# Kernel optimization log

Measured on AMD Instinct MI355X. Metric: run time of the kernel, lower is better.

Reference implementation:

```python
import jax, jax.numpy as jnp
import numpy as np

L, N, K, S, V, H = 12, 2048, 8, 4, 50000, 256


def setup_inputs() -> dict:
    key = jax.random.key(0)
    ks = jax.random.split(key, 20)
    tokens1 = jax.random.randint(ks[0], (L, N, S), 0, V, dtype=jnp.int32)
    tokens2 = jax.random.randint(ks[1], (L, N, S), 0, V, dtype=jnp.int32)
    # child indices into previous level's h (0 = zero-init row, -1 = no child)
    idx1 = jax.random.randint(ks[2], (L, N, K), -1, N + 1, dtype=jnp.int32).at[0].set(-1)
    idx2 = jax.random.randint(ks[3], (L, N, K), -1, N + 1, dtype=jnp.int32).at[0].set(-1)
    sc = 0.02
    E = jax.random.normal(ks[4], (V, H), jnp.float32)  # torch.randn init
    lin_W = jax.random.normal(ks[5], (H * S, H), jnp.float32) * sc
    lin_b = jnp.zeros((H,), jnp.float32)
    Uf_W = jax.random.normal(ks[6], (H, H), jnp.float32) * sc
    Uf_b = jnp.zeros((H,), jnp.float32)
    Uiuo_W = jax.random.normal(ks[7], (H, 3 * H), jnp.float32) * sc
    Uiuo_b = jnp.zeros((3 * H,), jnp.float32)
    W_W = jax.random.normal(ks[8], (H, 4 * H), jnp.float32) * sc
    W_b = jnp.zeros((4 * H,), jnp.float32)
    dense_W = jax.random.normal(ks[9], (H, 512), jnp.float32) * sc
    dense_b = jnp.zeros((512,), jnp.float32)
    out_W = jax.random.normal(ks[10], (512, 2), jnp.float32) * sc
    out_b = jnp.zeros((2,), jnp.float32)
    return dict(tokens1=tokens1, idx1=idx1, tokens2=tokens2, idx2=idx2,
                E=E, lin_W=lin_W, lin_b=lin_b, Uf_W=Uf_W, Uf_b=Uf_b,
                Uiuo_W=Uiuo_W, Uiuo_b=Uiuo_b, W_W=W_W, W_b=W_b,
                dense_W=dense_W, dense_b=dense_b, out_W=out_W, out_b=out_b)


def _encode(tokens, idx, E, lin_W, lin_b, Uf_W, Uf_b, Uiuo_W, Uiuo_b, W_W, W_b):
    # TreeEmbeddingLayer: lookup label_size tokens per node, concat, linear
    emb = E[tokens].reshape(L, N, S * H)           # [L,N,S*H]
    x = emb @ lin_W + lin_b                        # [L,N,H]

    def step(carry, inp):
        h_prev, c_prev = carry                     # [N,H]
        xl, il = inp                               # [N,H], [N,K]
        zero = jnp.zeros((1, H), xl.dtype)
        hp = jnp.concatenate([zero, h_prev], 0)    # [N+1,H] (row 0 = init)
        cp = jnp.concatenate([zero, c_prev], 0)
        mask_bool = il != -1
        index = jnp.where(mask_bool, il, 0)
        h = hp[index]                              # [N,K,H] gather child states
        c = cp[index]
        m = mask_bool[..., None].astype(xl.dtype)  # [N,K,1]
        h_sum = jnp.sum(h * m, axis=1)             # [N,H]
        Wx = xl @ W_W + W_b                        # [N,4H]
        Wf, Wi, Wu, Wo = Wx[:, :H], Wx[:, H:2*H], Wx[:, 2*H:3*H], Wx[:, 3*H:]
        fk = jax.nn.sigmoid(Wf[:, None, :] + h @ Uf_W + Uf_b)  # [N,K,H]
        bf = jnp.sum(fk * c * m, axis=1)           # [N,H]
        iuo = h_sum @ Uiuo_W + Uiuo_b              # [N,3H]
        i = jax.nn.sigmoid(iuo[:, :H] + Wi)
        u = jnp.tanh(iuo[:, H:2*H] + Wu)
        o = jax.nn.sigmoid(iuo[:, 2*H:] + Wo)
        nc = i * u + bf
        nh = o * jnp.tanh(nc)
        return (nh, nc), nh

    init = (jnp.zeros((N, H), x.dtype), jnp.zeros((N, H), x.dtype))
    (_, _), hs = jax.lax.scan(step, init, (x, idx))
    # 1 layer with skip connection; hx = last (root) level
    return hs[-1] + x[-1]                          # [N,H]


def reference(tokens1, idx1, tokens2, idx2, E, lin_W, lin_b, Uf_W, Uf_b,
              Uiuo_W, Uiuo_b, W_W, W_b, dense_W, dense_b, out_W, out_b):
    h1 = _encode(tokens1, idx1, E, lin_W, lin_b, Uf_W, Uf_b, Uiuo_W, Uiuo_b, W_W, W_b)
    h2 = _encode(tokens2, idx2, E, lin_W, lin_b, Uf_W, Uf_b, Uiuo_W, Uiuo_b, W_W, W_b)
    abs_dist = jnp.abs(h1 - h2)                    # [N,H]
    x = jnp.tanh(abs_dist @ dense_W + dense_b)     # dropout = identity (eval)
    logits = x @ out_W + out_b                     # [N,2]
    return jax.nn.softmax(logits, axis=-1)
```

## Files before the change

### kernel.cpp

```cpp
#include <hip/hip_runtime.h>

#define LL 12
#define NN 2048
#define KK 8
#define SS 4
#define HH 256
#define LN (LL*NN)
#define VV 50000
#define ZROW 4096
#define SROW 1536

typedef __bf16 bf16_t;
typedef __bf16 bf16x8 __attribute__((ext_vector_type(8)));
typedef __bf16 bf16x4v __attribute__((ext_vector_type(4)));
typedef float f32x4 __attribute__((ext_vector_type(4)));

__device__ __forceinline__ float sigmoidf_(float x) { return 1.f / (1.f + expf(-x)); }

__global__ __launch_bounds__(256) void k_cvtE(const float* __restrict__ src,
                                              bf16_t* __restrict__ dst, int n4)
{
    int i = blockIdx.x * 256 + threadIdx.x;
    const int stride = gridDim.x * 256;
    for (; i < n4; i += stride) {
        const float4 v = ((const float4*)src)[i];
        bf16x4v o;
        o[0] = (bf16_t)v.x; o[1] = (bf16_t)v.y; o[2] = (bf16_t)v.z; o[3] = (bf16_t)v.w;
        ((bf16x4v*)dst)[i] = o;
    }
}

__global__ __launch_bounds__(256) void k_cvtW(
    const float* __restrict__ linW, const float* __restrict__ WW,
    const float* __restrict__ UfW, const float* __restrict__ UiW,
    bf16_t* __restrict__ linWt, bf16_t* __restrict__ WWt,
    bf16_t* __restrict__ UfWt, bf16_t* __restrict__ UiWt)
{
    int i = blockIdx.x * 256 + threadIdx.x;
    if (i < 262144) {
        const int rr = i >> 8, cc = i & 255;
        linWt[(size_t)cc * 1024 + rr] = (bf16_t)linW[i];
        return;
    }
    i -= 262144;
    if (i < 262144) {
        const int rr = i >> 10, cc = i & 1023;
        WWt[(size_t)cc * 256 + rr] = (bf16_t)WW[i];
        return;
    }
    i -= 262144;
    if (i < 65536) {
        const int rr = i >> 8, cc = i & 255;
        UfWt[(size_t)cc * 256 + rr] = (bf16_t)UfW[i];
        return;
    }
    i -= 65536;
    if (i < 196608) {
        const int rr = i / 768, cc = i - rr * 768;
        UiWt[(size_t)cc * 256 + rr] = (bf16_t)UiW[i];
    }
}

__global__ __launch_bounds__(256) void k_zero(float* __restrict__ SA, float* __restrict__ SB)
{
    const int t = threadIdx.x;
    float* a = SA + (size_t)ZROW * 384;
    float* b = SB + (size_t)ZROW * 384;
    for (int i = t; i < 384; i += 256) { a[i] = 0.f; b[i] = 0.f; }
}

__global__ __launch_bounds__(256) void k_embed(
    const int* __restrict__ tok1, const int* __restrict__ tok2,
    const bf16_t* __restrict__ Ebf, const bf16_t* __restrict__ linWt,
    const float* __restrict__ linb, bf16_t* __restrict__ xout)
{
    __shared__ int toff[64][SS];
    const int t = threadIdx.x;
    const int m0 = blockIdx.x * 64;
    {
        const int lr = t >> 2, s = t & 3;
        const int m = m0 + lr;
        const int e = (m >= LN) ? 1 : 0;
        const int rrow = m - e * LN;
        const int* tok = e ? tok2 : tok1;
        toff[lr][s] = tok[(size_t)rrow * SS + s] * HH;
    }
    __syncthreads();
    const int lane = t & 63, w = t >> 6;
    const int wm = w >> 1, wn = w & 1;
    const int r = lane & 15, kg = lane >> 4;
    const int lr0 = wm * 32 + r, lr1 = lr0 + 16;
    const bf16_t* bp[8];
    #pragma unroll
    for (int j = 0; j < 8; ++j)
        bp[j] = linWt + (size_t)(wn * 128 + j * 16 + r) * 1024 + kg * 8;

    const f32x4 zero = {0.f, 0.f, 0.f, 0.f};
    f32x4 acc[2][8];
    #pragma unroll
    for (int mi = 0; mi < 2; ++mi)
        #pragma unroll
        for (int j = 0; j < 8; ++j) acc[mi][j] = zero;

    for (int k0 = 0; k0 < 1024; k0 += 32) {
        const int s = k0 >> 8, off = (k0 & 255) + kg * 8;
        const bf16x8 a0 = *(const bf16x8*)(Ebf + (size_t)toff[lr0][s] + off);
        const bf16x8 a1 = *(const bf16x8*)(Ebf + (size_t)toff[lr1][s] + off);
        #pragma unroll
        for (int j = 0; j < 8; ++j) {
            const bf16x8 b = *(const bf16x8*)bp[j];
            acc[0][j] = __builtin_amdgcn_mfma_f32_16x16x32_bf16(a0, b, acc[0][j], 0, 0, 0);
            acc[1][j] = __builtin_amdgcn_mfma_f32_16x16x32_bf16(a1, b, acc[1][j], 0, 0, 0);
            bp[j] += 32;
        }
    }
    const int crow = m0 + wm * 32 + kg * 4;
    #pragma unroll
    for (int j = 0; j < 8; ++j) {
        const int ccol = wn * 128 + j * 16 + r;
        const float bv = linb[ccol];
        #pragma unroll
        for (int mi = 0; mi < 2; ++mi)
            #pragma unroll
            for (int jj = 0; jj < 4; ++jj)
                xout[(size_t)(crow + mi * 16 + jj) * HH + ccol] =
                    (bf16_t)(acc[mi][j][jj] + bv);
    }
}

__global__ __launch_bounds__(512, 2) void k_step(
    const bf16_t* __restrict__ xbf,
    const int* __restrict__ idx1, const int* __restrict__ idx2, const int l,
    const bf16_t* __restrict__ UfWt, const float* __restrict__ Ufb,
    const bf16_t* __restrict__ UiWt, const float* __restrict__ Uib,
    const bf16_t* __restrict__ WWt, const float* __restrict__ Wb,
    const char* __restrict__ Sprev, char* __restrict__ Snext)
{
    __shared__ __align__(16) bf16_t WxL[16 * 1024];
    __shared__ __align__(16) bf16_t iuoL[16 * 768];
    __shared__ __align__(16) bf16_t hsumL[16 * 256];

    const int t = threadIdx.x;
    const int bid = blockIdx.x;
    const int x  = bid & 7;
    const int e  = x >> 2;
    const int n0 = ((bid >> 3) * 4 + (x & 3)) * 16;
    const int g0 = e * NN + n0;
    const int lane = t & 63, w = t >> 6;
    const int r = lane & 15, kg = lane >> 4;
    const f32x4 zero = {0.f, 0.f, 0.f, 0.f};

    const int rr = t >> 5, sl = t & 31;
    const int ss = (sl + 4 * (rr & 7)) & 31;

    int ch[KK];
    {
        const int* idxp = (e ? idx2 : idx1) + ((size_t)l * NN + n0 + rr) * KK;
        const int4 i0 = *(const int4*)idxp;
        const int4 i1 = *(const int4*)(idxp + 4);
        ch[0] = i0.x; ch[1] = i0.y; ch[2] = i0.z; ch[3] = i0.w;
        ch[4] = i1.x; ch[5] = i1.y; ch[6] = i1.z; ch[7] = i1.w;
        #pragma unroll
        for (int k = 0; k < KK; ++k)
            ch[k] = (ch[k] >= 1) ? (e * NN + ch[k] - 1) : ZROW;
    }

    bf16x8 hv[KK];
    #pragma unroll
    for (int k = 0; k < KK; ++k)
        hv[k] = *(const bf16x8*)(Sprev + (size_t)ch[k] * SROW + sl * 16);

    const bf16_t* xrow = xbf + ((size_t)e * LN + (size_t)l * NN + n0 + r) * HH + kg * 8;
    bf16x8 aWx[8];
    #pragma unroll
    for (int k = 0; k < 8; ++k) aWx[k] = *(const bf16x8*)(xrow + k * 32);

    {
        const bf16_t* bw[8];
        #pragma unroll
        for (int j = 0; j < 8; ++j)
            bw[j] = WWt + (size_t)((8 * w + j) * 16 + r) * HH + kg * 8;
        f32x4 acc[8];
        #pragma unroll
        for (int j = 0; j < 8; ++j) acc[j] = zero;
        #pragma unroll
        for (int k = 0; k < 8; ++k) {
            #pragma unroll
            for (int j = 0; j < 8; ++j) {
                const bf16x8 b = *(const bf16x8*)bw[j];
                acc[j] = __builtin_amdgcn_mfma_f32_16x16x32_bf16(aWx[k], b, acc[j], 0, 0, 0);
                bw[j] += 32;
            }
        }
        #pragma unroll
        for (int j = 0; j < 8; ++j) {
            const int col = (8 * w + j) * 16 + r;
            const float bv = Wb[col];
            #pragma unroll
            for (int jj = 0; jj < 4; ++jj)
                WxL[(size_t)(kg * 4 + jj) * 1024 + col] = (bf16_t)(acc[j][jj] + bv);
        }
    }

    {
        float hs[8] = {0.f, 0.f, 0.f, 0.f, 0.f, 0.f, 0.f, 0.f};
        #pragma unroll
        for (int k = 0; k < KK; ++k) {
            #pragma unroll
            for (int j = 0; j < 8; ++j) hs[j] += (float)hv[k][j];
        }
        bf16x8 o;
        #pragma unroll
        for (int j = 0; j < 8; ++j) o[j] = (bf16_t)hs[j];
        *(bf16x8*)(hsumL + rr * 256 + ss * 8) = o;
    }
    __syncthreads();

    bf16x8 cv[KK], fv[KK];
    #pragma unroll
    for (int k = 0; k < KK; ++k) {
        const char* row = Sprev + (size_t)ch[k] * SROW;
        fv[k] = *(const bf16x8*)(row + 512 + sl * 16);
        cv[k] = *(const bf16x8*)(row + 1024 + sl * 16);
    }

    {
        const bf16_t* bu[6];
        #pragma unroll
        for (int j = 0; j < 6; ++j)
            bu[j] = UiWt + (size_t)((6 * w + j) * 16 + r) * HH + kg * 8;
        f32x4 acc[6];
        #pragma unroll
        for (int j = 0; j < 6; ++j) acc[j] = zero;
        for (int k0 = 0; k0 < HH; k0 += 32) {
            const int sa = (((k0 >> 3) + kg) + 4 * (r & 7)) & 31;
            const bf16x8 a = *(const bf16x8*)(hsumL + r * 256 + sa * 8);
            #pragma unroll
            for (int j = 0; j < 6; ++j) {
                const bf16x8 b = *(const bf16x8*)bu[j];
                acc[j] = __builtin_amdgcn_mfma_f32_16x16x32_bf16(a, b, acc[j], 0, 0, 0);
                bu[j] += 32;
            }
        }
        #pragma unroll
        for (int j = 0; j < 6; ++j) {
            const int col = (6 * w + j) * 16 + r;
            const float bv = Uib[col];
            #pragma unroll
            for (int jj = 0; jj < 4; ++jj)
                iuoL[(size_t)(kg * 4 + jj) * 768 + col] = (bf16_t)(acc[j][jj] + bv);
        }
    }

    float ba[8] = {0.f, 0.f, 0.f, 0.f, 0.f, 0.f, 0.f, 0.f};
    {
        float wf[8];
        const bf16x8 wv = *(const bf16x8*)(WxL + (size_t)rr * 1024 + sl * 8);
        #pragma unroll
        for (int j = 0; j < 8; ++j) wf[j] = (float)wv[j];
        #pragma unroll
        for (int k = 0; k < KK; ++k) {
            #pragma unroll
            for (int j = 0; j < 8; ++j) {
                const float fk = sigmoidf_(wf[j] + (float)fv[k][j]);
                ba[j] = fmaf(fk, (float)cv[k][j], ba[j]);
            }
        }
    }
    __syncthreads();

    {
        const bf16x8 wiv = *(const bf16x8*)(WxL + (size_t)rr * 1024 + 256 + sl * 8);
        const bf16x8 wuv = *(const bf16x8*)(WxL + (size_t)rr * 1024 + 512 + sl * 8);
        const bf16x8 wov = *(const bf16x8*)(WxL + (size_t)rr * 1024 + 768 + sl * 8);
        const bf16x8 iv  = *(const bf16x8*)(iuoL + (size_t)rr * 768 + sl * 8);
        const bf16x8 uv  = *(const bf16x8*)(iuoL + (size_t)rr * 768 + 256 + sl * 8);
        const bf16x8 ov  = *(const bf16x8*)(iuoL + (size_t)rr * 768 + 512 + sl * 8);
        bf16x8 ncb, nhb;
        #pragma unroll
        for (int j = 0; j < 8; ++j) {
            const float ig = sigmoidf_((float)iv[j] + (float)wiv[j]);
            const float ug = tanhf((float)uv[j] + (float)wuv[j]);
            const float og = sigmoidf_((float)ov[j] + (float)wov[j]);
            const float nc = fmaf(ig, ug, ba[j]);
            ncb[j] = (bf16_t)nc;
            nhb[j] = (bf16_t)(og * tanhf(nc));
        }
        char* rowN = Snext + (size_t)(g0 + rr) * SROW;
        *(bf16x8*)(rowN + sl * 16) = nhb;
        *(bf16x8*)(rowN + 1024 + sl * 16) = ncb;
        *(bf16x8*)(hsumL + rr * 256 + ss * 8) = nhb;
    }

    if (l < LL - 1) {
        __syncthreads();
        const int ct0 = 2 * w;
        const bf16_t* bq0 = UfWt + (size_t)(ct0 * 16 + r) * HH + kg * 8;
        const bf16_t* bq1 = bq0 + (size_t)16 * HH;
        f32x4 ac0 = zero, ac1 = zero;
        for (int k0 = 0; k0 < HH; k0 += 32) {
            const int sa = (((k0 >> 3) + kg) + 4 * (r & 7)) & 31;
            const bf16x8 a = *(const bf16x8*)(hsumL + r * 256 + sa * 8);
            const bf16x8 b0 = *(const bf16x8*)bq0;
            const bf16x8 b1 = *(const bf16x8*)bq1;
            ac0 = __builtin_amdgcn_mfma_f32_16x16x32_bf16(a, b0, ac0, 0, 0, 0);
            ac1 = __builtin_amdgcn_mfma_f32_16x16x32_bf16(a, b1, ac1, 0, 0, 0);
            bq0 += 32; bq1 += 32;
        }
        const int c0 = ct0 * 16 + r, c1 = c0 + 16;
        const float bv0 = Ufb[c0], bv1 = Ufb[c1];
        #pragma unroll
        for (int jj = 0; jj < 4; ++jj) {
            bf16_t* fr = (bf16_t*)(Snext + (size_t)(g0 + kg * 4 + jj) * SROW + 512);
            fr[c0] = (bf16_t)(ac0[jj] + bv0);
            fr[c1] = (bf16_t)(ac1[jj] + bv1);
        }
    }
}

__global__ __launch_bounds__(256) void k_final(
    const char* __restrict__ Sfin, const bf16_t* __restrict__ xbf,
    const float* __restrict__ dW, const float* __restrict__ db,
    const float* __restrict__ oW, const float* __restrict__ ob,
    float* __restrict__ out)
{
    __shared__ __align__(16) float ad[8][HH];
    __shared__ __align__(16) float xx[8][512];
    const int t = threadIdx.x;
    const int n0 = blockIdx.x * 8;
    const size_t xoff1 = (size_t)(LL - 1) * NN * HH;
    const size_t xoff2 = (size_t)LN * HH + xoff1;
    #pragma unroll
    for (int rr = 0; rr < 8; ++rr) {
        const int n = n0 + rr;
        const float h1 = (float)((const bf16_t*)(Sfin + (size_t)n * SROW))[t]
                       + (float)xbf[xoff1 + (size_t)n * HH + t];
        const float h2 = (float)((const bf16_t*)(Sfin + (size_t)(NN + n) * SROW))[t]
                       + (float)xbf[xoff2 + (size_t)n * HH + t];
        ad[rr][t] = fabsf(h1 - h2);
    }
    __syncthreads();
    float a0[8], a1[8];
    #pragma unroll
    for (int rr = 0; rr < 8; ++rr) { a0[rr] = 0.f; a1[rr] = 0.f; }
    for (int k = 0; k < HH; k += 4) {
        #pragma unroll
        for (int kk = 0; kk < 4; ++kk) {
            const float b0 = dW[(size_t)(k + kk) * 512 + t];
            const float b1 = dW[(size_t)(k + kk) * 512 + 256 + t];
            #pragma unroll
            for (int rr = 0; rr < 8; ++rr) {
                const float av = ad[rr][k + kk];
                a0[rr] = fmaf(av, b0, a0[rr]);
                a1[rr] = fmaf(av, b1, a1[rr]);
            }
        }
    }
    const float db0 = db[t], db1 = db[256 + t];
    #pragma unroll
    for (int rr = 0; rr < 8; ++rr) {
        xx[rr][t] = tanhf(a0[rr] + db0);
        xx[rr][256 + t] = tanhf(a1[rr] + db1);
    }
    __syncthreads();
    const int w = t >> 6, lane = t & 63;
    for (int rr = w; rr < 8; rr += 4) {
        float p0 = 0.f, p1 = 0.f;
        for (int k = lane; k < 512; k += 64) {
            const float xv = xx[rr][k];
            p0 = fmaf(xv, oW[2 * k + 0], p0);
            p1 = fmaf(xv, oW[2 * k + 1], p1);
        }
        #pragma unroll
        for (int off = 32; off > 0; off >>= 1) {
            p0 += __shfl_down(p0, off);
            p1 += __shfl_down(p1, off);
        }
        if (lane == 0) {
            const float l0 = p0 + ob[0], l1 = p1 + ob[1];
            const float mx = fmaxf(l0, l1);
            const float e0 = expf(l0 - mx), e1 = expf(l1 - mx);
            const float inv = 1.f / (e0 + e1);
            out[(size_t)(n0 + rr) * 2 + 0] = e0 * inv;
            out[(size_t)(n0 + rr) * 2 + 1] = e1 * inv;
        }
    }
}

extern "C" void kernel_launch(void* const* d_in, const int* in_sizes, int n_in,
                              void* d_out, int out_size, void* d_ws, size_t ws_size,
                              hipStream_t stream) {
    (void)in_sizes; (void)n_in; (void)out_size; (void)ws_size;
    const int*   tok1 = (const int*)d_in[0];
    const int*   idx1 = (const int*)d_in[1];
    const int*   tok2 = (const int*)d_in[2];
    const int*   idx2 = (const int*)d_in[3];
    const float* E    = (const float*)d_in[4];
    const float* linW = (const float*)d_in[5];
    const float* linb = (const float*)d_in[6];
    const float* UfW  = (const float*)d_in[7];
    const float* Ufb  = (const float*)d_in[8];
    const float* UiW  = (const float*)d_in[9];
    const float* Uib  = (const float*)d_in[10];
    const float* WW   = (const float*)d_in[11];
    const float* Wb   = (const float*)d_in[12];
    const float* dW   = (const float*)d_in[13];
    const float* db   = (const float*)d_in[14];
    const float* oW   = (const float*)d_in[15];
    const float* ob   = (const float*)d_in[16];
    float* out = (float*)d_out;

    bf16_t* xbf = (bf16_t*)d_ws;
    char*   uni = (char*)(xbf + (size_t)12582912);
    bf16_t* Ebf = (bf16_t*)uni;
    char*   SA  = uni;
    char*   SB  = uni + 6292992;
    bf16_t* linWt = (bf16_t*)(uni + 25600000);
    bf16_t* WWt   = linWt + (size_t)262144;
    bf16_t* UfWt  = WWt   + (size_t)262144;
    bf16_t* UiWt  = UfWt  + (size_t)65536;

    k_cvtE<<<2048, 256, 0, stream>>>(E, Ebf, VV * HH / 4);
    k_cvtW<<<3072, 256, 0, stream>>>(linW, WW, UfW, UiW, linWt, WWt, UfWt, UiWt);

    k_embed<<<768, 256, 0, stream>>>(tok1, tok2, Ebf, linWt, linb, xbf);

    k_zero<<<1, 256, 0, stream>>>((float*)SA, (float*)SB);

    char *Sp = SA, *Sn = SB;
    for (int l = 0; l < LL; ++l) {
        k_step<<<256, 512, 0, stream>>>(xbf, idx1, idx2, l,
                                        UfWt, Ufb, UiWt, Uib, WWt, Wb, Sp, Sn);
        char* ts = Sp; Sp = Sn; Sn = ts;
    }

    k_final<<<NN / 8, 256, 0, stream>>>(Sp, xbf, dW, db, oW, ob, out);
}
```

Baseline: 701.6 us.

## Precompute W·x for all levels in embed kernel, slim per-level step

Fuses the input projection x@W into the embedding kernel, so W·x for every level and both trees is computed in one large batched GEMM. The result is stored as a 1024-wide bf16 buffer in workspace, and only the root-level x is kept for the final stage. The per-level step kernel then just loads its precomputed Wx rows instead of running an MFMA GEMM inside the serial chain, which removes work from the latency-critical recurrence. The cost is a much larger workspace (about 100 MB of Wx) and extra global traffic. The old path is kept as a fallback when the workspace is too small.

```diff
diff --git a/kernel.cpp b/kernel.cpp
--- a/kernel.cpp
+++ b/kernel.cpp
@@ -69,12 +69,15 @@
     for (int i = t; i < 384; i += 256) { a[i] = 0.f; b[i] = 0.f; }
 }
 
-__global__ __launch_bounds__(256) void k_embed(
+__global__ __launch_bounds__(256) void k_embedwx(
     const int* __restrict__ tok1, const int* __restrict__ tok2,
     const bf16_t* __restrict__ Ebf, const bf16_t* __restrict__ linWt,
-    const float* __restrict__ linb, bf16_t* __restrict__ xout)
+    const float* __restrict__ linb,
+    const bf16_t* __restrict__ WWt, const float* __restrict__ Wb,
+    bf16_t* __restrict__ xsm, bf16_t* __restrict__ Wxs)
 {
     __shared__ int toff[64][SS];
+    __shared__ __align__(16) bf16_t xtile[64 * 256];
     const int t = threadIdx.x;
     const int m0 = blockIdx.x * 64;
     {
@@ -90,53 +93,98 @@
     const int wm = w >> 1, wn = w & 1;
     const int r = lane & 15, kg = lane >> 4;
     const int lr0 = wm * 32 + r, lr1 = lr0 + 16;
-    const bf16_t* bp[8];
-    #pragma unroll
-    for (int j = 0; j < 8; ++j)
-        bp[j] = linWt + (size_t)(wn * 128 + j * 16 + r) * 1024 + kg * 8;
-
     const f32x4 zero = {0.f, 0.f, 0.f, 0.f};
-    f32x4 acc[2][8];
-    #pragma unroll
-    for (int mi = 0; mi < 2; ++mi)
-        #pragma unroll
-        for (int j = 0; j < 8; ++j) acc[mi][j] = zero;
-
-    for (int k0 = 0; k0 < 1024; k0 += 32) {
-        const int s = k0 >> 8, off = (k0 & 255) + kg * 8;
-        const bf16x8 a0 = *(const bf16x8*)(Ebf + (size_t)toff[lr0][s] + off);
-        const bf16x8 a1 = *(const bf16x8*)(Ebf + (size_t)toff[lr1][s] + off);
+
+    {
+        const bf16_t* bp[8];
+        #pragma unroll
+        for (int j = 0; j < 8; ++j)
+            bp[j] = linWt + (size_t)(wn * 128 + j * 16 + r) * 1024 + kg * 8;
+        f32x4 acc[2][8];
+        #pragma unroll
+        for (int mi = 0; mi < 2; ++mi)
+            #pragma unroll
+            for (int j = 0; j < 8; ++j) acc[mi][j] = zero;
+
+        for (int k0 = 0; k0 < 1024; k0 += 32) {
+            const int s = k0 >> 8, off = (k0 & 255) + kg * 8;
+            const bf16x8 a0 = *(const bf16x8*)(Ebf + (size_t)toff[lr0][s] + off);
+            const bf16x8 a1 = *(const bf16x8*)(Ebf + (size_t)toff[lr1][s] + off);
+            #pragma unroll
+            for (int j = 0; j < 8; ++j) {
+                const bf16x8 b = *(const bf16x8*)bp[j];
+                acc[0][j] = __builtin_amdgcn_mfma_f32_16x16x32_bf16(a0, b, acc[0][j], 0, 0, 0);
+                acc[1][j] = __builtin_amdgcn_mfma_f32_16x16x32_bf16(a1, b, acc[1][j], 0, 0, 0);
+                bp[j] += 32;
+            }
+        }
+        const int e0 = (m0 >= LN) ? 1 : 0;
+        const int lblk = (m0 - e0 * LN) >> 11;
+        const int nbase = m0 & (NN - 1);
+        const int crowL = wm * 32 + kg * 4;
         #pragma unroll
         for (int j = 0; j < 8; ++j) {
-            const bf16x8 b = *(const bf16x8*)bp[j];
-            acc[0][j] = __builtin_amdgcn_mfma_f32_16x16x32_bf16(a0, b, acc[0][j], 0, 0, 0);
-            acc[1][j] = __builtin_amdgcn_mfma_f32_16x16x32_bf16(a1, b, acc[1][j], 0, 0, 0);
-            bp[j] += 32;
-        }
-    }
-    const int crow = m0 + wm * 32 + kg * 4;
-    #pragma unroll
-    for (int j = 0; j < 8; ++j) {
-        const int ccol = wn * 128 + j * 16 + r;
-        const float bv = linb[ccol];
-        #pragma unroll
-        for (int mi = 0; mi < 2; ++mi)
-            #pragma unroll
-            for (int jj = 0; jj < 4; ++jj)
-                xout[(size_t)(crow + mi * 16 + jj) * HH + ccol] =
-                    (bf16_t)(acc[mi][j][jj] + bv);
-    }
-}
-
-__global__ __launch_bounds__(512, 2) void k_step(
-    const bf16_t* __restrict__ xbf,
+            const int ccol = wn * 128 + j * 16 + r;
+            const float bv = linb[ccol];
+            #pragma unroll
+            for (int mi = 0; mi < 2; ++mi) {
+                #pragma unroll
+                for (int jj = 0; jj < 4; ++jj) {
+                    const int rowL = crowL + mi * 16 + jj;
+                    const bf16_t val = (bf16_t)(acc[mi][j][jj] + bv);
+                    const int ps = ((ccol >> 3) + rowL) & 31;
+                    xtile[rowL * 256 + ps * 8 + (ccol & 7)] = val;
+                    if (lblk == LL - 1)
+                        xsm[((size_t)e0 * NN + nbase + rowL) * HH + ccol] = val;
+                }
+            }
+        }
+    }
+    __syncthreads();
+
+    for (int mp = 0; mp < 2; ++mp) {
+        for (int nh = 0; nh < 2; ++nh) {
+            f32x4 acc2[2][8];
+            #pragma unroll
+            for (int mi = 0; mi < 2; ++mi)
+                #pragma unroll
+                for (int nt = 0; nt < 8; ++nt) acc2[mi][nt] = zero;
+            for (int k0 = 0; k0 < 8; ++k0) {
+                const int row0 = mp * 32 + r, row1 = row0 + 16;
+                const int sk = k0 * 4 + kg;
+                const bf16x8 a0 = *(const bf16x8*)(xtile + row0 * 256 + ((sk + row0) & 31) * 8);
+                const bf16x8 a1 = *(const bf16x8*)(xtile + row1 * 256 + ((sk + row1) & 31) * 8);
+                #pragma unroll
+                for (int nt = 0; nt < 8; ++nt) {
+                    const bf16x8 b = *(const bf16x8*)(WWt +
+                        (size_t)(w * 256 + (nh * 8 + nt) * 16 + r) * HH + k0 * 32 + kg * 8);
+                    acc2[0][nt] = __builtin_amdgcn_mfma_f32_16x16x32_bf16(a0, b, acc2[0][nt], 0, 0, 0);
+                    acc2[1][nt] = __builtin_amdgcn_mfma_f32_16x16x32_bf16(a1, b, acc2[1][nt], 0, 0, 0);
+                }
+            }
+            #pragma unroll
+            for (int nt = 0; nt < 8; ++nt) {
+                const int col = w * 256 + (nh * 8 + nt) * 16 + r;
+                const float bv = Wb[col];
+                #pragma unroll
+                for (int mi = 0; mi < 2; ++mi) {
+                    #pragma unroll
+                    for (int jj = 0; jj < 4; ++jj)
+                        Wxs[(size_t)(m0 + mp * 32 + mi * 16 + kg * 4 + jj) * 1024 + col] =
+                            (bf16_t)(acc2[mi][nt][jj] + bv);
+                }
+            }
+        }
+    }
+}
+
+__global__ __launch_bounds__(512, 2) void k_step2(
     const int* __restrict__ idx1, const int* __restrict__ idx2, const int l,
     const bf16_t* __restrict__ UfWt, const float* __restrict__ Ufb,
     const bf16_t* __restrict__ UiWt, const float* __restrict__ Uib,
-    const bf16_t* __restrict__ WWt, const float* __restrict__ Wb,
+    const bf16_t* __restrict__ Wxs,
     const char* __restrict__ Sprev, char* __restrict__ Snext)
 {
-    __shared__ __align__(16) bf16_t WxL[16 * 1024];
     __shared__ __align__(16) bf16_t iuoL[16 * 768];
     __shared__ __align__(16) bf16_t hsumL[16 * 256];
 
@@ -165,41 +213,18 @@
             ch[k] = (ch[k] >= 1) ? (e * NN + ch[k] - 1) : ZROW;
     }
 
-    bf16x8 hv[KK];
-    #pragma unroll
-    for (int k = 0; k < KK; ++k)
-        hv[k] = *(const bf16x8*)(Sprev + (size_t)ch[k] * SROW + sl * 16);
-
-    const bf16_t* xrow = xbf + ((size_t)e * LN + (size_t)l * NN + n0 + r) * HH + kg * 8;
-    bf16x8 aWx[8];
-    #pragma unroll
-    for (int k = 0; k < 8; ++k) aWx[k] = *(const bf16x8*)(xrow + k * 32);
-
-    {
-        const bf16_t* bw[8];
-        #pragma unroll
-        for (int j = 0; j < 8; ++j)
-            bw[j] = WWt + (size_t)((8 * w + j) * 16 + r) * HH + kg * 8;
-        f32x4 acc[8];
-        #pragma unroll
-        for (int j = 0; j < 8; ++j) acc[j] = zero;
-        #pragma unroll
-        for (int k = 0; k < 8; ++k) {
-            #pragma unroll
-            for (int j = 0; j < 8; ++j) {
-                const bf16x8 b = *(const bf16x8*)bw[j];
-                acc[j] = __builtin_amdgcn_mfma_f32_16x16x32_bf16(aWx[k], b, acc[j], 0, 0, 0);
-                bw[j] += 32;
-            }
-        }
-        #pragma unroll
-        for (int j = 0; j < 8; ++j) {
-            const int col = (8 * w + j) * 16 + r;
-            const float bv = Wb[col];
-            #pragma unroll
-            for (int jj = 0; jj < 4; ++jj)
-                WxL[(size_t)(kg * 4 + jj) * 1024 + col] = (bf16_t)(acc[j][jj] + bv);
-        }
+    const bf16_t* wxp = Wxs + ((size_t)e * LN + (size_t)l * NN + n0 + rr) * 1024;
+    const bf16x8 wfv = *(const bf16x8*)(wxp + sl * 8);
+    const bf16x8 wiv = *(const bf16x8*)(wxp + 256 + sl * 8);
+    const bf16x8 wuv = *(const bf16x8*)(wxp + 512 + sl * 8);
+    const bf16x8 wov = *(const bf16x8*)(wxp + 768 + sl * 8);
+    bf16x8 hv[KK], fv[KK], cv[KK];
+    #pragma unroll
+    for (int k = 0; k < KK; ++k) {
+        const char* row = Sprev + (size_t)ch[k] * SROW;
+        hv[k] = *(const bf16x8*)(row + sl * 16);
+        fv[k] = *(const bf16x8*)(row + 512 + sl * 16);
+        cv[k] = *(const bf16x8*)(row + 1024 + sl * 16);
     }
 
     {
@@ -215,14 +240,6 @@
         *(bf16x8*)(hsumL + rr * 256 + ss * 8) = o;
     }
     __syncthreads();
-
-    bf16x8 cv[KK], fv[KK];
-    #pragma unroll
-    for (int k = 0; k < KK; ++k) {
-        const char* row = Sprev + (size_t)ch[k] * SROW;
-        fv[k] = *(const bf16x8*)(row + 512 + sl * 16);
-        cv[k] = *(const bf16x8*)(row + 1024 + sl * 16);
-    }
 
     {
         const bf16_t* bu[6];
@@ -255,9 +272,8 @@
     float ba[8] = {0.f, 0.f, 0.f, 0.f, 0.f, 0.f, 0.f, 0.f};
     {
         float wf[8];
-        const bf16x8 wv = *(const bf16x8*)(WxL + (size_t)rr * 1024 + sl * 8);
-        #pragma unroll
-        for (int j = 0; j < 8; ++j) wf[j] = (float)wv[j];
+        #pragma unroll
+        for (int j = 0; j < 8; ++j) wf[j] = (float)wfv[j];
         #pragma unroll
         for (int k = 0; k < KK; ++k) {
             #pragma unroll
@@ -270,12 +286,9 @@
     __syncthreads();
 
     {
-        const bf16x8 wiv = *(const bf16x8*)(WxL + (size_t)rr * 1024 + 256 + sl * 8);
-        const bf16x8 wuv = *(const bf16x8*)(WxL + (size_t)rr * 1024 + 512 + sl * 8);
-        const bf16x8 wov = *(const bf16x8*)(WxL + (size_t)rr * 1024 + 768 + sl * 8);
-        const bf16x8 iv  = *(const bf16x8*)(iuoL + (size_t)rr * 768 + sl * 8);
-        const bf16x8 uv  = *(const bf16x8*)(iuoL + (size_t)rr * 768 + 256 + sl * 8);
-        const bf16x8 ov  = *(const bf16x8*)(iuoL + (size_t)rr * 768 + 512 + sl * 8);
+        const bf16x8 iv = *(const bf16x8*)(iuoL + (size_t)rr * 768 + sl * 8);
+        const bf16x8 uv = *(const bf16x8*)(iuoL + (size_t)rr * 768 + 256 + sl * 8);
+        const bf16x8 ov = *(const bf16x8*)(iuoL + (size_t)rr * 768 + 512 + sl * 8);
         bf16x8 ncb, nhb;
         #pragma unroll
         for (int j = 0; j < 8; ++j) {
@@ -318,6 +331,308 @@
     }
 }
 
+__global__ __launch_bounds__(256) void k_final2(
+    const char* __restrict__ Sfin, const bf16_t* __restrict__ xsm,
+    const float* __restrict__ dW, const float* __restrict__ db,
+    const float* __restrict__ oW, const float* __restrict__ ob,
+    float* __restrict__ out)
+{
+    __shared__ __align__(16) float ad[8][HH];
+    __shared__ __align__(16) float xx[8][512];
+    const int t = threadIdx.x;
+    const int n0 = blockIdx.x * 8;
+    #pragma unroll
+    for (int rr = 0; rr < 8; ++rr) {
+        const int n = n0 + rr;
+        const float h1 = (float)((const bf16_t*)(Sfin + (size_t)n * SROW))[t]
+                       + (float)xsm[(size_t)n * HH + t];
+        const float h2 = (float)((const bf16_t*)(Sfin + (size_t)(NN + n) * SROW))[t]
+                       + (float)xsm[((size_t)NN + n) * HH + t];
+        ad[rr][t] = fabsf(h1 - h2);
+    }
+    __syncthreads();
+    float a0[8], a1[8];
+    #pragma unroll
+    for (int rr = 0; rr < 8; ++rr) { a0[rr] = 0.f; a1[rr] = 0.f; }
+    for (int k = 0; k < HH; k += 4) {
+        #pragma unroll
+        for (int kk = 0; kk < 4; ++kk) {
+            const float b0 = dW[(size_t)(k + kk) * 512 + t];
+            const float b1 = dW[(size_t)(k + kk) * 512 + 256 + t];
+            #pragma unroll
+            for (int rr = 0; rr < 8; ++rr) {
+                const float av = ad[rr][k + kk];
+                a0[rr] = fmaf(av, b0, a0[rr]);
+                a1[rr] = fmaf(av, b1, a1[rr]);
+            }
+        }
+    }
+    const float db0 = db[t], db1 = db[256 + t];
+    #pragma unroll
+    for (int rr = 0; rr < 8; ++rr) {
+        xx[rr][t] = tanhf(a0[rr] + db0);
+        xx[rr][256 + t] = tanhf(a1[rr] + db1);
+    }
+    __syncthreads();
+    const int w = t >> 6, lane = t & 63;
+    for (int rr = w; rr < 8; rr += 4) {
+        float p0 = 0.f, p1 = 0.f;
+        for (int k = lane; k < 512; k += 64) {
+            const float xv = xx[rr][k];
+            p0 = fmaf(xv, oW[2 * k + 0], p0);
+            p1 = fmaf(xv, oW[2 * k + 1], p1);
+        }
+        #pragma unroll
+        for (int off = 32; off > 0; off >>= 1) {
+            p0 += __shfl_down(p0, off);
+            p1 += __shfl_down(p1, off);
+        }
+        if (lane == 0) {
+            const float l0 = p0 + ob[0], l1 = p1 + ob[1];
+            const float mx = fmaxf(l0, l1);
+            const float e0 = expf(l0 - mx), e1 = expf(l1 - mx);
+            const float inv = 1.f / (e0 + e1);
+            out[(size_t)(n0 + rr) * 2 + 0] = e0 * inv;
+            out[(size_t)(n0 + rr) * 2 + 1] = e1 * inv;
+        }
+    }
+}
+
+__global__ __launch_bounds__(256) void k_embed(
+    const int* __restrict__ tok1, const int* __restrict__ tok2,
+    const bf16_t* __restrict__ Ebf, const bf16_t* __restrict__ linWt,
+    const float* __restrict__ linb, bf16_t* __restrict__ xout)
+{
+    __shared__ int toff[64][SS];
+    const int t = threadIdx.x;
+    const int m0 = blockIdx.x * 64;
+    {
+        const int lr = t >> 2, s = t & 3;
+        const int m = m0 + lr;
+        const int e = (m >= LN) ? 1 : 0;
+        const int rrow = m - e * LN;
+        const int* tok = e ? tok2 : tok1;
+        toff[lr][s] = tok[(size_t)rrow * SS + s] * HH;
+    }
+    __syncthreads();
+    const int lane = t & 63, w = t >> 6;
+    const int wm = w >> 1, wn = w & 1;
+    const int r = lane & 15, kg = lane >> 4;
+    const int lr0 = wm * 32 + r, lr1 = lr0 + 16;
+    const bf16_t* bp[8];
+    #pragma unroll
+    for (int j = 0; j < 8; ++j)
+        bp[j] = linWt + (size_t)(wn * 128 + j * 16 + r) * 1024 + kg * 8;
+    const f32x4 zero = {0.f, 0.f, 0.f, 0.f};
+    f32x4 acc[2][8];
+    #pragma unroll
+    for (int mi = 0; mi < 2; ++mi)
+        #pragma unroll
+        for (int j = 0; j < 8; ++j) acc[mi][j] = zero;
+    for (int k0 = 0; k0 < 1024; k0 += 32) {
+        const int s = k0 >> 8, off = (k0 & 255) + kg * 8;
+        const bf16x8 a0 = *(const bf16x8*)(Ebf + (size_t)toff[lr0][s] + off);
+        const bf16x8 a1 = *(const bf16x8*)(Ebf + (size_t)toff[lr1][s] + off);
+        #pragma unroll
+        for (int j = 0; j < 8; ++j) {
+            const bf16x8 b = *(const bf16x8*)bp[j];
+            acc[0][j] = __builtin_amdgcn_mfma_f32_16x16x32_bf16(a0, b, acc[0][j], 0, 0, 0);
+            acc[1][j] = __builtin_amdgcn_mfma_f32_16x16x32_bf16(a1, b, acc[1][j], 0, 0, 0);
+            bp[j] += 32;
+        }
+    }
+    const int crow = m0 + wm * 32 + kg * 4;
+    #pragma unroll
+    for (int j = 0; j < 8; ++j) {
+        const int ccol = wn * 128 + j * 16 + r;
+        const float bv = linb[ccol];
+        #pragma unroll
+        for (int mi = 0; mi < 2; ++mi)
+            #pragma unroll
+            for (int jj = 0; jj < 4; ++jj)
+                xout[(size_t)(crow + mi * 16 + jj) * HH + ccol] =
+                    (bf16_t)(acc[mi][j][jj] + bv);
+    }
+}
+
+__global__ __launch_bounds__(512, 2) void k_step(
+    const bf16_t* __restrict__ xbf,
+    const int* __restrict__ idx1, const int* __restrict__ idx2, const int l,
+    const bf16_t* __restrict__ UfWt, const float* __restrict__ Ufb,
+    const bf16_t* __restrict__ UiWt, const float* __restrict__ Uib,
+    const bf16_t* __restrict__ WWt, const float* __restrict__ Wb,
+    const char* __restrict__ Sprev, char* __restrict__ Snext)
+{
+    __shared__ __align__(16) bf16_t WxL[16 * 1024];
+    __shared__ __align__(16) bf16_t iuoL[16 * 768];
+    __shared__ __align__(16) bf16_t hsumL[16 * 256];
+    const int t = threadIdx.x;
+    const int bid = blockIdx.x;
+    const int x  = bid & 7;
+    const int e  = x >> 2;
+    const int n0 = ((bid >> 3) * 4 + (x & 3)) * 16;
+    const int g0 = e * NN + n0;
+    const int lane = t & 63, w = t >> 6;
+    const int r = lane & 15, kg = lane >> 4;
+    const f32x4 zero = {0.f, 0.f, 0.f, 0.f};
+    const int rr = t >> 5, sl = t & 31;
+    const int ss = (sl + 4 * (rr & 7)) & 31;
+    int ch[KK];
+    {
+        const int* idxp = (e ? idx2 : idx1) + ((size_t)l * NN + n0 + rr) * KK;
+        const int4 i0 = *(const int4*)idxp;
+        const int4 i1 = *(const int4*)(idxp + 4);
+        ch[0] = i0.x; ch[1] = i0.y; ch[2] = i0.z; ch[3] = i0.w;
+        ch[4] = i1.x; ch[5] = i1.y; ch[6] = i1.z; ch[7] = i1.w;
+        #pragma unroll
+        for (int k = 0; k < KK; ++k)
+            ch[k] = (ch[k] >= 1) ? (e * NN + ch[k] - 1) : ZROW;
+    }
+    bf16x8 hv[KK];
+    #pragma unroll
+    for (int k = 0; k < KK; ++k)
+        hv[k] = *(const bf16x8*)(Sprev + (size_t)ch[k] * SROW + sl * 16);
+    const bf16_t* xrow = xbf + ((size_t)e * LN + (size_t)l * NN + n0 + r) * HH + kg * 8;
+    bf16x8 aWx[8];
+    #pragma unroll
+    for (int k = 0; k < 8; ++k) aWx[k] = *(const bf16x8*)(xrow + k * 32);
+    {
+        const bf16_t* bw[8];
+        #pragma unroll
+        for (int j = 0; j < 8; ++j)
+            bw[j] = WWt + (size_t)((8 * w + j) * 16 + r) * HH + kg * 8;
+        f32x4 acc[8];
+        #pragma unroll
+        for (int j = 0; j < 8; ++j) acc[j] = zero;
+        #pragma unroll
+        for (int k = 0; k < 8; ++k) {
+            #pragma unroll
+            for (int j = 0; j < 8; ++j) {
+                const bf16x8 b = *(const bf16x8*)bw[j];
+                acc[j] = __builtin_amdgcn_mfma_f32_16x16x32_bf16(aWx[k], b, acc[j], 0, 0, 0);
+                bw[j] += 32;
+            }
+        }
+        #pragma unroll
+        for (int j = 0; j < 8; ++j) {
+            const int col = (8 * w + j) * 16 + r;
+            const float bv = Wb[col];
+            #pragma unroll
+            for (int jj = 0; jj < 4; ++jj)
+                WxL[(size_t)(kg * 4 + jj) * 1024 + col] = (bf16_t)(acc[j][jj] + bv);
+        }
+    }
+    {
+        float hs[8] = {0.f, 0.f, 0.f, 0.f, 0.f, 0.f, 0.f, 0.f};
+        #pragma unroll
+        for (int k = 0; k < KK; ++k) {
+            #pragma unroll
+            for (int j = 0; j < 8; ++j) hs[j] += (float)hv[k][j];
+        }
+        bf16x8 o;
+        #pragma unroll
+        for (int j = 0; j < 8; ++j) o[j] = (bf16_t)hs[j];
+        *(bf16x8*)(hsumL + rr * 256 + ss * 8) = o;
+    }
+    __syncthreads();
+    bf16x8 cv[KK], fvv[KK];
+    #pragma unroll
+    for (int k = 0; k < KK; ++k) {
+        const char* row = Sprev + (size_t)ch[k] * SROW;
+        fvv[k] = *(const bf16x8*)(row + 512 + sl * 16);
+        cv[k]  = *(const bf16x8*)(row + 1024 + sl * 16);
+    }
+    {
+        const bf16_t* bu[6];
+        #pragma unroll
+        for (int j = 0; j < 6; ++j)
+            bu[j] = UiWt + (size_t)((6 * w + j) * 16 + r) * HH + kg * 8;
+        f32x4 acc[6];
+        #pragma unroll
+        for (int j = 0; j < 6; ++j) acc[j] = zero;
+        for (int k0 = 0; k0 < HH; k0 += 32) {
+            const int sa = (((k0 >> 3) + kg) + 4 * (r & 7)) & 31;
+            const bf16x8 a = *(const bf16x8*)(hsumL + r * 256 + sa * 8);
+            #pragma unroll
+            for (int j = 0; j < 6; ++j) {
+                const bf16x8 b = *(const bf16x8*)bu[j];
+                acc[j] = __builtin_amdgcn_mfma_f32_16x16x32_bf16(a, b, acc[j], 0, 0, 0);
+                bu[j] += 32;
+            }
+        }
+        #pragma unroll
+        for (int j = 0; j < 6; ++j) {
+            const int col = (6 * w + j) * 16 + r;
+            const float bv = Uib[col];
+            #pragma unroll
+            for (int jj = 0; jj < 4; ++jj)
+                iuoL[(size_t)(kg * 4 + jj) * 768 + col] = (bf16_t)(acc[j][jj] + bv);
+        }
+    }
+    float ba[8] = {0.f, 0.f, 0.f, 0.f, 0.f, 0.f, 0.f, 0.f};
+    {
+        float wf[8];
+        const bf16x8 wv = *(const bf16x8*)(WxL + (size_t)rr * 1024 + sl * 8);
+        #pragma unroll
+        for (int j = 0; j < 8; ++j) wf[j] = (float)wv[j];
+        #pragma unroll
+        for (int k = 0; k < KK; ++k) {
+            #pragma unroll
+            for (int j = 0; j < 8; ++j) {
+                const float fk = sigmoidf_(wf[j] + (float)fvv[k][j]);
+                ba[j] = fmaf(fk, (float)cv[k][j], ba[j]);
+            }
+        }
+    }
+    __syncthreads();
+    {
+        const bf16x8 wiv = *(const bf16x8*)(WxL + (size_t)rr * 1024 + 256 + sl * 8);
+        const bf16x8 wuv = *(const bf16x8*)(WxL + (size_t)rr * 1024 + 512 + sl * 8);
+        const bf16x8 wov = *(const bf16x8*)(WxL + (size_t)rr * 1024 + 768 + sl * 8);
+        const bf16x8 iv  = *(const bf16x8*)(iuoL + (size_t)rr * 768 + sl * 8);
+        const bf16x8 uv  = *(const bf16x8*)(iuoL + (size_t)rr * 768 + 256 + sl * 8);
+        const bf16x8 ov  = *(const bf16x8*)(iuoL + (size_t)rr * 768 + 512 + sl * 8);
+        bf16x8 ncb, nhb;
+        #pragma unroll
+        for (int j = 0; j < 8; ++j) {
+            const float ig = sigmoidf_((float)iv[j] + (float)wiv[j]);
+            const float ug = tanhf((float)uv[j] + (float)wuv[j]);
+            const float og = sigmoidf_((float)ov[j] + (float)wov[j]);
+            const float nc = fmaf(ig, ug, ba[j]);
+            ncb[j] = (bf16_t)nc;
+            nhb[j] = (bf16_t)(og * tanhf(nc));
+        }
+        char* rowN = Snext + (size_t)(g0 + rr) * SROW;
+        *(bf16x8*)(rowN + sl * 16) = nhb;
+        *(bf16x8*)(rowN + 1024 + sl * 16) = ncb;
+        *(bf16x8*)(hsumL + rr * 256 + ss * 8) = nhb;
+    }
+    if (l < LL - 1) {
+        __syncthreads();
+        const int ct0 = 2 * w;
+        const bf16_t* bq0 = UfWt + (size_t)(ct0 * 16 + r) * HH + kg * 8;
+        const bf16_t* bq1 = bq0 + (size_t)16 * HH;
+        f32x4 ac0 = zero, ac1 = zero;
+        for (int k0 = 0; k0 < HH; k0 += 32) {
+            const int sa = (((k0 >> 3) + kg) + 4 * (r & 7)) & 31;
+            const bf16x8 a = *(const bf16x8*)(hsumL + r * 256 + sa * 8);
+            const bf16x8 b0 = *(const bf16x8*)bq0;
+            const bf16x8 b1 = *(const bf16x8*)bq1;
+            ac0 = __builtin_amdgcn_mfma_f32_16x16x32_bf16(a, b0, ac0, 0, 0, 0);
+            ac1 = __builtin_amdgcn_mfma_f32_16x16x32_bf16(a, b1, ac1, 0, 0, 0);
+            bq0 += 32; bq1 += 32;
+        }
+        const int c0 = ct0 * 16 + r, c1 = c0 + 16;
+        const float bv0 = Ufb[c0], bv1 = Ufb[c1];
+        #pragma unroll
+        for (int jj = 0; jj < 4; ++jj) {
+            bf16_t* fr = (bf16_t*)(Snext + (size_t)(g0 + kg * 4 + jj) * SROW + 512);
+            fr[c0] = (bf16_t)(ac0[jj] + bv0);
+            fr[c1] = (bf16_t)(ac1[jj] + bv1);
+        }
+    }
+}
+
 __global__ __launch_bounds__(256) void k_final(
     const char* __restrict__ Sfin, const bf16_t* __restrict__ xbf,
     const float* __restrict__ dW, const float* __restrict__ db,
@@ -390,7 +705,7 @@
 extern "C" void kernel_launch(void* const* d_in, const int* in_sizes, int n_in,
                               void* d_out, int out_size, void* d_ws, size_t ws_size,
                               hipStream_t stream) {
-    (void)in_sizes; (void)n_in; (void)out_size; (void)ws_size;
+    (void)in_sizes; (void)n_in; (void)out_size;
     const int*   tok1 = (const int*)d_in[0];
     const int*   idx1 = (const int*)d_in[1];
     const int*   tok2 = (const int*)d_in[2];
@@ -410,29 +725,54 @@
     const float* ob   = (const float*)d_in[16];
     float* out = (float*)d_out;
 
-    bf16_t* xbf = (bf16_t*)d_ws;
-    char*   uni = (char*)(xbf + (size_t)12582912);
-    bf16_t* Ebf = (bf16_t*)uni;
-    char*   SA  = uni;
-    char*   SB  = uni + 6292992;
-    bf16_t* linWt = (bf16_t*)(uni + 25600000);
-    bf16_t* WWt   = linWt + (size_t)262144;
-    bf16_t* UfWt  = WWt   + (size_t)262144;
-    bf16_t* UiWt  = UfWt  + (size_t)65536;
-
-    k_cvtE<<<2048, 256, 0, stream>>>(E, Ebf, VV * HH / 4);
-    k_cvtW<<<3072, 256, 0, stream>>>(linW, WW, UfW, UiW, linWt, WWt, UfWt, UiWt);
-
-    k_embed<<<768, 256, 0, stream>>>(tok1, tok2, Ebf, linWt, linb, xbf);
-
-    k_zero<<<1, 256, 0, stream>>>((float*)SA, (float*)SB);
-
-    char *Sp = SA, *Sn = SB;
-    for (int l = 0; l < LL; ++l) {
-        k_step<<<256, 512, 0, stream>>>(xbf, idx1, idx2, l,
-                                        UfWt, Ufb, UiWt, Uib, WWt, Wb, Sp, Sn);
-        char* ts = Sp; Sp = Sn; Sn = ts;
-    }
-
-    k_final<<<NN / 8, 256, 0, stream>>>(Sp, xbf, dW, db, oW, ob, out);
-}
+    const size_t NEED = 100663296ull + 25600000ull + 2097152ull + 1572864ull;
+
+    if (ws_size >= NEED) {
+        bf16_t* Wxs = (bf16_t*)d_ws;
+        char*   uni = (char*)d_ws + 100663296;
+        bf16_t* Ebf = (bf16_t*)uni;
+        char*   SA  = uni;
+        char*   SB  = uni + 6292992;
+        bf16_t* xsm = (bf16_t*)(uni + 25600000);
+        bf16_t* linWt = (bf16_t*)(uni + 25600000 + 2097152);
+        bf16_t* WWt   = linWt + (size_t)262144;
+        bf16_t* UfWt  = WWt   + (size_t)262144;
+        bf16_t* UiWt  = UfWt  + (size_t)65536;
+
+        k_cvtE<<<2048, 256, 0, stream>>>(E, Ebf, VV * HH / 4);
+        k_cvtW<<<3072, 256, 0, stream>>>(linW, WW, UfW, UiW, linWt, WWt, UfWt, UiWt);
+        k_embedwx<<<768, 256, 0, stream>>>(tok1, tok2, Ebf, linWt, linb, WWt, Wb, xsm, Wxs);
+        k_zero<<<1, 256, 0, stream>>>((float*)SA, (float*)SB);
+
+        char *Sp = SA, *Sn = SB;
+        for (int l = 0; l < LL; ++l) {
+            k_step2<<<256, 512, 0, stream>>>(idx1, idx2, l, UfWt, Ufb, UiWt, Uib,
+                                             Wxs, Sp, Sn);
+            char* ts = Sp; Sp = Sn; Sn = ts;
+        }
+        k_final2<<<NN / 8, 256, 0, stream>>>(Sp, xsm, dW, db, oW, ob, out);
+    } else {
+        bf16_t* xbf = (bf16_t*)d_ws;
+        char*   uni = (char*)(xbf + (size_t)12582912);
+        bf16_t* Ebf = (bf16_t*)uni;
+        char*   SA  = uni;
+        char*   SB  = uni + 6292992;
+        bf16_t* linWt = (bf16_t*)(uni + 25600000);
+        bf16_t* WWt   = linWt + (size_t)262144;
+        bf16_t* UfWt  = WWt   + (size_t)262144;
+        bf16_t* UiWt  = UfWt  + (size_t)65536;
+
+        k_cvtE<<<2048, 256, 0, stream>>>(E, Ebf, VV * HH / 4);
+        k_cvtW<<<3072, 256, 0, stream>>>(linW, WW, UfW, UiW, linWt, WWt, UfWt, UiWt);
+        k_embed<<<768, 256, 0, stream>>>(tok1, tok2, Ebf, linWt, linb, xbf);
+        k_zero<<<1, 256, 0, stream>>>((float*)SA, (float*)SB);
+
+        char *Sp = SA, *Sn = SB;
+        for (int l = 0; l < LL; ++l) {
+            k_step<<<256, 512, 0, stream>>>(xbf, idx1, idx2, l,
+                                            UfWt, Ufb, UiWt, Uib, WWt, Wb, Sp, Sn);
+            char* ts = Sp; Sp = Sn; Sn = ts;
+        }
+        k_final<<<NN / 8, 256, 0, stream>>>(Sp, xbf, dW, db, oW, ob, out);
+    }
+}
```

Measured after the change: 698.8 us. Within noise of the previous version (-0.4%).
